# Kernel tuning notes

Measured on AMD Instinct MI355X. Metric: run time of the kernel, lower is better.

## Reference

```python
import jax, jax.numpy as jnp
import numpy as np

H = 1024
V = 32000
L = 15
B = 512


def setup_inputs() -> dict:
    key = jax.random.key(0)
    ks = jax.random.split(key, 16)
    s = 0.02
    return {
        "input_ids": jax.random.randint(ks[0], (B,), 0, V),
        "hidden": jax.random.normal(ks[1], (1, B, H), jnp.float32),
        "encoder_outputs": jax.random.normal(ks[2], (L, B, H), jnp.float32),
        "max_length": L,
        "embedding": jax.random.normal(ks[3], (V, H), jnp.float32) * s,
        "attn1_w": jax.random.normal(ks[4], (1, 2 * H), jnp.float32) * s,
        "attn1_b": jnp.zeros((1,), jnp.float32),
        "combine_w": jax.random.normal(ks[5], (H, 2 * H), jnp.float32) * s,
        "combine_b": jnp.zeros((H,), jnp.float32),
        "w_ih": jax.random.normal(ks[6], (3 * H, H), jnp.float32) * s,
        "w_hh": jax.random.normal(ks[7], (3 * H, H), jnp.float32) * s,
        "b_ih": jnp.zeros((3 * H,), jnp.float32),
        "b_hh": jnp.zeros((3 * H,), jnp.float32),
        "out_w": jax.random.normal(ks[8], (V, H), jnp.float32) * s,
        "out_b": jnp.zeros((V,), jnp.float32),
    }


def reference(input_ids, hidden, encoder_outputs, max_length, embedding,
              attn1_w, attn1_b, combine_w, combine_b,
              w_ih, w_hh, b_ih, b_hh, out_w, out_b):
    # embedding lookup (dropout is identity in eval mode)
    emb = embedding[input_ids]                       # [B, H]
    # Bahdanau-style additive scores: vectorize the per-step python loop
    emb_l = jnp.broadcast_to(emb[None], (max_length, B, H))   # [L, B, H]
    cat = jnp.concatenate([emb_l, encoder_outputs], axis=-1)  # [L, B, 2H]
    scores = cat @ attn1_w.T + attn1_b               # [L, B, 1]
    attn_weights = jax.nn.softmax(scores, axis=0)    # softmax over L
    ctx = jnp.sum(attn_weights * encoder_outputs, axis=0)     # [B, H]
    x = jnp.concatenate([emb, ctx], axis=-1) @ combine_w.T + combine_b  # [B, H]
    # n_layers = 1: relu then one GRU step (seq len 1)
    x = jax.nn.relu(x)
    h = hidden[0]                                    # [B, H]
    gi = x @ w_ih.T + b_ih                           # [B, 3H]
    gh = h @ w_hh.T + b_hh                           # [B, 3H]
    i_r, i_z, i_n = jnp.split(gi, 3, axis=1)
    h_r, h_z, h_n = jnp.split(gh, 3, axis=1)
    r = jax.nn.sigmoid(i_r + h_r)
    z = jax.nn.sigmoid(i_z + h_z)
    n = jnp.tanh(i_n + r * h_n)
    h_new = (1.0 - z) * n + z * h                    # [B, H]
    logits = h_new @ out_w.T + out_b                 # [B, V]
    output = jax.nn.log_softmax(logits, axis=1)
    return output, h_new[None], attn_weights
```

## Files before the change

### kernel.cpp

```cpp
#include <hip/hip_runtime.h>

#define HH 1024
#define VV 32000
#define LL 15
#define BB 512

typedef __bf16 bf16;
typedef __bf16 bf16x4 __attribute__((ext_vector_type(4)));
typedef __bf16 bf16x8 __attribute__((ext_vector_type(8)));
typedef float f32x4 __attribute__((ext_vector_type(4)));

__device__ __forceinline__ unsigned short f2bf(float f) {
    unsigned int u = __float_as_uint(f);
    unsigned int r = (u + 0x7fffu + ((u >> 16) & 1u)) >> 16;
    return (unsigned short)r;
}

__device__ __forceinline__ void gld_lds16(const void* g, void* l) {
    __builtin_amdgcn_global_load_lds(
        (const __attribute__((address_space(1))) unsigned int*)g,
        (__attribute__((address_space(3))) unsigned int*)l, 16, 0, 0);
}

__global__ __launch_bounds__(256)
void cvt4_kernel(const float* __restrict__ a0, unsigned short* __restrict__ o0, int n0_,
                 const float* __restrict__ a1, unsigned short* __restrict__ o1, int n1_,
                 const float* __restrict__ a2, unsigned short* __restrict__ o2, int n2_,
                 const float* __restrict__ a3, unsigned short* __restrict__ o3, int n3_) {
    int i = blockIdx.x * 256 + threadIdx.x;
    const float* src; unsigned short* dst;
    if (i < n0_) { src = a0; dst = o0; }
    else if ((i -= n0_) < n1_) { src = a1; dst = o1; }
    else if ((i -= n1_) < n2_) { src = a2; dst = o2; }
    else if ((i -= n2_) < n3_) { src = a3; dst = o3; }
    else return;
    const f32x4 a = ((const f32x4*)src)[2 * i], b = ((const f32x4*)src)[2 * i + 1];
    ((bf16x4*)dst)[2 * i]     = __builtin_convertvector(a, bf16x4);
    ((bf16x4*)dst)[2 * i + 1] = __builtin_convertvector(b, bf16x4);
}

__global__ __launch_bounds__(256)
void attn_kernel(const int* __restrict__ ids, const float* __restrict__ enc,
                 const float* __restrict__ embedding,
                 const float* __restrict__ attn1_w, const float* __restrict__ attn1_b,
                 float* __restrict__ attn_out, unsigned short* __restrict__ cat_out) {
    const int b = blockIdx.x, tid = threadIdx.x;
    const int lane = tid & 63, wv = tid >> 6;

    __shared__ float s_enc[LL * HH];
    __shared__ float s_scores[LL];
    __shared__ float s_red[4];

    for (int idx = tid; idx < LL * HH / 4; idx += 256) {
        const int l = (idx * 4) >> 10, h = (idx * 4) & (HH - 1);
        *(f32x4*)&s_enc[idx * 4] = *(const f32x4*)&enc[((size_t)l * BB + b) * HH + h];
    }

    const float* embr = embedding + (size_t)ids[b] * HH;
    float p = 0.f;
    for (int j = tid; j < HH; j += 256) p += embr[j] * attn1_w[j];
    #pragma unroll
    for (int o = 32; o; o >>= 1) p += __shfl_xor(p, o);
    if (lane == 0) s_red[wv] = p;
    __syncthreads();
    const float semb = s_red[0] + s_red[1] + s_red[2] + s_red[3] + attn1_b[0];

    for (int l = wv; l < LL; l += 4) {
        float q = 0.f;
        for (int j = lane; j < HH; j += 64) q += s_enc[l * HH + j] * attn1_w[HH + j];
        #pragma unroll
        for (int o = 32; o; o >>= 1) q += __shfl_xor(q, o);
        if (lane == 0) s_scores[l] = q + semb;
    }
    __syncthreads();

    float mx = -3.4e38f;
    #pragma unroll
    for (int l = 0; l < LL; l++) mx = fmaxf(mx, s_scores[l]);
    float aw[LL], sum = 0.f;
    #pragma unroll
    for (int l = 0; l < LL; l++) { aw[l] = __expf(s_scores[l] - mx); sum += aw[l]; }
    const float inv = 1.f / sum;
    #pragma unroll
    for (int l = 0; l < LL; l++) aw[l] *= inv;

    if (tid < LL) attn_out[tid * BB + b] = aw[tid];

    for (int j = tid; j < HH; j += 256) {
        float c = 0.f;
        #pragma unroll
        for (int l = 0; l < LL; l++) c += aw[l] * s_enc[l * HH + j];
        cat_out[(size_t)b * (2 * HH) + j] = f2bf(embr[j]);
        cat_out[(size_t)b * (2 * HH) + HH + j] = f2bf(c);
    }
}

template<int TM, int TN, int OUT, int GATES>
__global__ __launch_bounds__(256)
void gemm_nt(const bf16* __restrict__ A, const bf16* __restrict__ B,
             const float* __restrict__ bias, void* __restrict__ Cout,
             const bf16* __restrict__ A2, const bf16* __restrict__ B2,
             const float* __restrict__ bias2, void* __restrict__ C2,
             const int K, const int N) {
    constexpr int FM = TM / 32, FN = TN / 32;
    __shared__ bf16 As[TM * 64];
    __shared__ bf16 Bs[TN * 64];

    if (GATES && blockIdx.z == 1) { A = A2; B = B2; bias = bias2; Cout = C2; }

    const int tid = threadIdx.x;
    const int lane = tid & 63, wave = tid >> 6;
    const int wm = wave >> 1, wn = wave & 1;
    const int rlo = lane & 15, khi = lane >> 4;
    const int m0 = blockIdx.y * TM, n0 = blockIdx.x * TN;

    f32x4 acc[FM][FN] = {};
    constexpr int IA = TM / 32, IB = TN / 32;

    for (int k0 = 0; k0 < K; k0 += 64) {
        #pragma unroll
        for (int i = 0; i < IA; i++) {
            const int t = (i * 256 + tid) * 8;
            gld_lds16(A + (size_t)(m0 + (t >> 6)) * K + (k0 + (t & 63)), As + i * 2048 + wave * 512);
        }
        #pragma unroll
        for (int i = 0; i < IB; i++) {
            const int t = (i * 256 + tid) * 8;
            gld_lds16(B + (size_t)(n0 + (t >> 6)) * K + (k0 + (t & 63)), Bs + i * 2048 + wave * 512);
        }
        __syncthreads();

        bf16x8 af[FM][2], bfr[FN][2];
        #pragma unroll
        for (int m = 0; m < FM; m++)
            #pragma unroll
            for (int ks = 0; ks < 2; ks++)
                af[m][ks] = *(const bf16x8*)(As + (wm * (TM / 2) + m * 16 + rlo) * 64 + ks * 32 + khi * 8);
        #pragma unroll
        for (int n = 0; n < FN; n++)
            #pragma unroll
            for (int ks = 0; ks < 2; ks++)
                bfr[n][ks] = *(const bf16x8*)(Bs + (wn * (TN / 2) + n * 16 + rlo) * 64 + ks * 32 + khi * 8);
        #pragma unroll
        for (int ks = 0; ks < 2; ks++)
            #pragma unroll
            for (int m = 0; m < FM; m++)
                #pragma unroll
                for (int n = 0; n < FN; n++)
                    acc[m][n] = __builtin_amdgcn_mfma_f32_16x16x32_bf16(af[m][ks], bfr[n][ks], acc[m][n], 0, 0, 0);
        __syncthreads();
    }

    #pragma unroll
    for (int m = 0; m < FM; m++) {
        const int gr = m0 + wm * (TM / 2) + m * 16 + khi * 4;
        #pragma unroll
        for (int n = 0; n < FN; n++) {
            const int gc = n0 + wn * (TN / 2) + n * 16 + rlo;
            const float bv = bias[gc];
            #pragma unroll
            for (int j = 0; j < 4; j++) {
                float v = acc[m][n][j] + bv;
                if (OUT == 1) {
                    v = fmaxf(v, 0.f);
                    ((unsigned short*)Cout)[(size_t)(gr + j) * N + gc] = f2bf(v);
                } else {
                    ((float*)Cout)[(size_t)(gr + j) * N + gc] = v;
                }
            }
        }
    }
}

__global__ __launch_bounds__(256, 3)
void gemm_out(const bf16* __restrict__ A, const float* __restrict__ B,
              const float* __restrict__ bias, float* __restrict__ C,
              float* __restrict__ pmax, float* __restrict__ psum) {
    constexpr int K = HH, N = VV;
    __shared__ bf16 As[128 * 64];
    __shared__ bf16 Bs[64 * 64];
    __shared__ float sPm[2][128], sPs[2][128];

    const int tid = threadIdx.x;
    const int lane = tid & 63, wave = tid >> 6;
    const int wm = wave >> 1, wn = wave & 1;
    const int rlo = lane & 15, khi = lane >> 4;

    constexpr int gridN = VV / 64;
    constexpr int nFull = (gridN >> 3) << 5;
    const int bidx = blockIdx.x;
    int g, jm;
    if (bidx < nFull) { const int s = bidx >> 5, rem = bidx & 31; jm = rem >> 3; g = s * 8 + (rem & 7); }
    else { const int rem = bidx - nFull; constexpr int gleft = gridN & 7; g = (gridN & ~7) + rem % gleft; jm = rem / gleft; }
    const int n0 = g * 64, m0 = jm * 128;

    f32x4 acc[4][2] = {};

    for (int k0 = 0; k0 < K; k0 += 64) {
        f32x4 bv[4];
        #pragma unroll
        for (int i = 0; i < 4; i++) {
            const int idx = i * 256 + tid;
            const int row = idx >> 4, c4 = idx & 15;
            bv[i] = *(const f32x4*)(B + (size_t)(n0 + row) * K + k0 + c4 * 4);
        }
        #pragma unroll
        for (int i = 0; i < 4; i++) {
            const int p = (i * 256 + tid) * 16;
            const int row = p >> 7;
            const int qs = (p & 127) ^ ((row & 7) << 4);
            gld_lds16(A + (size_t)(m0 + row) * K + k0 + (qs >> 1),
                      As + i * 2048 + wave * 512);
        }
        #pragma unroll
        for (int i = 0; i < 4; i++) {
            const int idx = i * 256 + tid;
            const int row = idx >> 4, c4 = idx & 15;
            bf16x4 w = __builtin_convertvector(bv[i], bf16x4);
            *(bf16x4*)((char*)Bs + row * 128 + ((c4 * 8) ^ ((row & 7) << 4))) = w;
        }
        __syncthreads();

        #pragma unroll
        for (int ks = 0; ks < 2; ks++) {
            bf16x8 af[4], bfr[2];
            #pragma unroll
            for (int m = 0; m < 4; m++) {
                const int r = wm * 64 + m * 16 + rlo;
                const int sw = (ks * 64 + khi * 16) ^ ((r & 7) << 4);
                af[m] = *(const bf16x8*)((const char*)As + r * 128 + sw);
            }
            #pragma unroll
            for (int n = 0; n < 2; n++) {
                const int r = wn * 32 + n * 16 + rlo;
                const int sw = (ks * 64 + khi * 16) ^ ((r & 7) << 4);
                bfr[n] = *(const bf16x8*)((const char*)Bs + r * 128 + sw);
            }
            #pragma unroll
            for (int m = 0; m < 4; m++)
                #pragma unroll
                for (int n = 0; n < 2; n++)
                    acc[m][n] = __builtin_amdgcn_mfma_f32_16x16x32_bf16(af[m], bfr[n], acc[m][n], 0, 0, 0);
        }
        __syncthreads();
    }

    float bvn[2];
    #pragma unroll
    for (int n = 0; n < 2; n++) bvn[n] = bias[n0 + wn * 32 + n * 16 + rlo];

    #pragma unroll
    for (int m = 0; m < 4; m++) {
        const int rbase = wm * 64 + m * 16 + khi * 4;
        #pragma unroll
        for (int j = 0; j < 4; j++) {
            const int gr = m0 + rbase + j;
            float v[2];
            #pragma unroll
            for (int n = 0; n < 2; n++) {
                v[n] = acc[m][n][j] + bvn[n];
                C[(size_t)gr * N + n0 + wn * 32 + n * 16 + rlo] = v[n];
            }
            float lm = fmaxf(v[0], v[1]);
            #pragma unroll
            for (int o = 8; o; o >>= 1) lm = fmaxf(lm, __shfl_xor(lm, o));
            float ls = __expf(v[0] - lm) + __expf(v[1] - lm);
            #pragma unroll
            for (int o = 8; o; o >>= 1) ls += __shfl_xor(ls, o);
            if (rlo == 0) { sPm[wn][rbase + j] = lm; sPs[wn][rbase + j] = ls; }
        }
    }
    __syncthreads();
    if (tid < 128) {
        const float ma = sPm[0][tid], mb = sPm[1][tid];
        const float M = fmaxf(ma, mb);
        const float S = sPs[0][tid] * __expf(ma - M) + sPs[1][tid] * __expf(mb - M);
        pmax[(size_t)(m0 + tid) * 512 + g] = M;
        psum[(size_t)(m0 + tid) * 512 + g] = S;
    }
}

__global__ __launch_bounds__(256)
void gru_kernel(const float* __restrict__ gi, const float* __restrict__ gh,
                const float* __restrict__ h, float* __restrict__ hnew,
                unsigned short* __restrict__ hnew_bf) {
    const int i = blockIdx.x * 256 + threadIdx.x;
    const int e = i * 4;
    const int b = e >> 10, j = e & (HH - 1);
    const size_t o = ((size_t)b * 3 * HH + j) / 4;
    const f32x4 ir = ((const f32x4*)gi)[o],          iz = ((const f32x4*)gi)[o + HH / 4],
                in_ = ((const f32x4*)gi)[o + 2 * HH / 4];
    const f32x4 hr = ((const f32x4*)gh)[o],          hz = ((const f32x4*)gh)[o + HH / 4],
                hn = ((const f32x4*)gh)[o + 2 * HH / 4];
    const f32x4 hv = ((const f32x4*)h)[i];
    f32x4 out;
    ushort4 ob;
    #pragma unroll
    for (int c = 0; c < 4; c++) {
        const float r = 1.f / (1.f + __expf(-(ir[c] + hr[c])));
        const float z = 1.f / (1.f + __expf(-(iz[c] + hz[c])));
        const float n = tanhf(in_[c] + r * hn[c]);
        const float v = (1.f - z) * n + z * hv[c];
        out[c] = v;
        ((unsigned short*)&ob)[c] = f2bf(v);
    }
    ((f32x4*)hnew)[i] = out;
    ((ushort4*)hnew_bf)[i] = ob;
}

__global__ __launch_bounds__(512)
void lsm_final(const float* __restrict__ pmax, const float* __restrict__ psum,
               float* __restrict__ logits) {
    const int b = blockIdx.x, tid = threadIdx.x;
    const int lane = tid & 63, wv = tid >> 6;
    __shared__ float sm[8], ss[8];

    float m = -3.4e38f, s = 0.f;
    if (tid < VV / 64) { m = pmax[(size_t)b * 512 + tid]; s = psum[(size_t)b * 512 + tid]; }
    #pragma unroll
    for (int o = 32; o; o >>= 1) {
        const float mo = __shfl_xor(m, o), so = __shfl_xor(s, o);
        const float nm = fmaxf(m, mo);
        s = s * __expf(m - nm) + so * __expf(mo - nm);
        m = nm;
    }
    if (lane == 0) { sm[wv] = m; ss[wv] = s; }
    __syncthreads();
    float M = sm[0], S;
    #pragma unroll
    for (int w = 1; w < 8; w++) M = fmaxf(M, sm[w]);
    S = ss[0] * __expf(sm[0] - M);
    #pragma unroll
    for (int w = 1; w < 8; w++) S += ss[w] * __expf(sm[w] - M);
    const float lse = M + __logf(S);

    float* row = logits + (size_t)b * VV;
    for (int j = tid; j < VV / 4; j += 512) {
        f32x4 v = ((const f32x4*)row)[j];
        v[0] -= lse; v[1] -= lse; v[2] -= lse; v[3] -= lse;
        ((f32x4*)row)[j] = v;
    }
}

extern "C" void kernel_launch(void* const* d_in, const int* in_sizes, int n_in,
                              void* d_out, int out_size, void* d_ws, size_t ws_size,
                              hipStream_t stream) {
    const int*   ids       = (const int*)d_in[0];
    const float* hidden    = (const float*)d_in[1];
    const float* enc       = (const float*)d_in[2];
    const float* embedding = (const float*)d_in[4];
    const float* attn1_w   = (const float*)d_in[5];
    const float* attn1_b   = (const float*)d_in[6];
    const float* combine_w = (const float*)d_in[7];
    const float* combine_b = (const float*)d_in[8];
    const float* w_ih      = (const float*)d_in[9];
    const float* w_hh      = (const float*)d_in[10];
    const float* b_ih      = (const float*)d_in[11];
    const float* b_hh      = (const float*)d_in[12];
    const float* out_w     = (const float*)d_in[13];
    const float* out_b     = (const float*)d_in[14];

    float* out_lsm = (float*)d_out;
    float* out_h   = out_lsm + (size_t)BB * VV;
    float* out_aw  = out_h + (size_t)BB * HH;

    char* w = (char*)d_ws;
    unsigned short* w_ih_bf  = (unsigned short*)w;   w += (size_t)3 * HH * HH * 2;
    unsigned short* w_hh_bf  = (unsigned short*)w;   w += (size_t)3 * HH * HH * 2;
    unsigned short* w_cb_bf  = (unsigned short*)w;   w += (size_t)2 * HH * HH * 2;
    unsigned short* cat_bf   = (unsigned short*)w;   w += (size_t)BB * 2 * HH * 2;
    unsigned short* x_bf     = (unsigned short*)w;   w += (size_t)BB * HH * 2;
    unsigned short* hid_bf   = (unsigned short*)w;   w += (size_t)BB * HH * 2;
    unsigned short* hnew_bf  = (unsigned short*)w;   w += (size_t)BB * HH * 2;
    float* gi   = (float*)w;                         w += (size_t)BB * 3 * HH * 4;
    float* gh   = (float*)w;                         w += (size_t)BB * 3 * HH * 4;
    float* pmax = (float*)w;                         w += (size_t)BB * 512 * 4;
    float* psum = (float*)w;                         w += (size_t)BB * 512 * 4;

    cvt4_kernel<<<(3 * HH * HH / 8 * 2 + 2 * HH * HH / 8 + BB * HH / 8) / 256, 256, 0, stream>>>(
        w_ih, w_ih_bf, 3 * HH * HH / 8,
        w_hh, w_hh_bf, 3 * HH * HH / 8,
        combine_w, w_cb_bf, 2 * HH * HH / 8,
        hidden, hid_bf, BB * HH / 8);

    attn_kernel<<<BB, 256, 0, stream>>>(ids, enc, embedding, attn1_w, attn1_b, out_aw, cat_bf);

    gemm_nt<64, 64, 1, 0><<<dim3(HH / 64, BB / 64), 256, 0, stream>>>(
        (const bf16*)cat_bf, (const bf16*)w_cb_bf, combine_b, x_bf,
        nullptr, nullptr, nullptr, nullptr, 2 * HH, HH);

    gemm_nt<64, 64, 0, 1><<<dim3(3 * HH / 64, BB / 64, 2), 256, 0, stream>>>(
        (const bf16*)hid_bf, (const bf16*)w_hh_bf, b_hh, gh,
        (const bf16*)x_bf, (const bf16*)w_ih_bf, b_ih, gi, HH, 3 * HH);

    gru_kernel<<<(BB * HH / 4) / 256, 256, 0, stream>>>(gi, gh, hidden, out_h, hnew_bf);

    gemm_out<<<(VV / 64) * 4, 256, 0, stream>>>(
        (const bf16*)hnew_bf, out_w, out_b, out_lsm, pmax, psum);

    lsm_final<<<BB, 512, 0, stream>>>(pmax, psum, out_lsm);
}
```

Measured before the change: 183.0 us.

## Double-buffer LDS tiles in gemm_nt and gemm_out to overlap loads with MFMA

Both GEMM kernels now use two LDS buffers per operand, so the next K-tile is prefetched while the current tile is being multiplied. This cuts the loop to one barrier per iteration. gemm_out also register-prefetches its fp32 B tile two steps ahead and converts it to bf16 after compute. gemm_nt additionally switches its A/B LDS layout to an XOR swizzle to reduce bank conflicts. The cost is doubled LDS use and more registers, which may lower occupancy (gemm_out keeps launch bounds of 3 blocks).

```diff
diff --git a/kernel.cpp b/kernel.cpp
--- a/kernel.cpp
+++ b/kernel.cpp
@@ -103,8 +103,8 @@
              const float* __restrict__ bias2, void* __restrict__ C2,
              const int K, const int N) {
     constexpr int FM = TM / 32, FN = TN / 32;
-    __shared__ bf16 As[TM * 64];
-    __shared__ bf16 Bs[TN * 64];
+    __shared__ bf16 As[2][TM * 64];
+    __shared__ bf16 Bs[2][TN * 64];
 
     if (GATES && blockIdx.z == 1) { A = A2; B = B2; bias = bias2; Cout = C2; }
 
@@ -117,38 +117,58 @@
     f32x4 acc[FM][FN] = {};
     constexpr int IA = TM / 32, IB = TN / 32;
 
-    for (int k0 = 0; k0 < K; k0 += 64) {
+    auto stage = [&](int k0, int buf) {
         #pragma unroll
         for (int i = 0; i < IA; i++) {
-            const int t = (i * 256 + tid) * 8;
-            gld_lds16(A + (size_t)(m0 + (t >> 6)) * K + (k0 + (t & 63)), As + i * 2048 + wave * 512);
+            const int p = (i * 256 + tid) * 16;
+            const int row = p >> 7;
+            const int qs = (p & 127) ^ ((row & 7) << 4);
+            gld_lds16(A + (size_t)(m0 + row) * K + k0 + (qs >> 1),
+                      &As[buf][0] + i * 2048 + wave * 512);
         }
         #pragma unroll
         for (int i = 0; i < IB; i++) {
-            const int t = (i * 256 + tid) * 8;
-            gld_lds16(B + (size_t)(n0 + (t >> 6)) * K + (k0 + (t & 63)), Bs + i * 2048 + wave * 512);
-        }
-        __syncthreads();
-
-        bf16x8 af[FM][2], bfr[FN][2];
-        #pragma unroll
-        for (int m = 0; m < FM; m++)
-            #pragma unroll
-            for (int ks = 0; ks < 2; ks++)
-                af[m][ks] = *(const bf16x8*)(As + (wm * (TM / 2) + m * 16 + rlo) * 64 + ks * 32 + khi * 8);
-        #pragma unroll
-        for (int n = 0; n < FN; n++)
-            #pragma unroll
-            for (int ks = 0; ks < 2; ks++)
-                bfr[n][ks] = *(const bf16x8*)(Bs + (wn * (TN / 2) + n * 16 + rlo) * 64 + ks * 32 + khi * 8);
-        #pragma unroll
-        for (int ks = 0; ks < 2; ks++)
+            const int p = (i * 256 + tid) * 16;
+            const int row = p >> 7;
+            const int qs = (p & 127) ^ ((row & 7) << 4);
+            gld_lds16(B + (size_t)(n0 + row) * K + k0 + (qs >> 1),
+                      &Bs[buf][0] + i * 2048 + wave * 512);
+        }
+    };
+
+    auto compute = [&](int buf) {
+        #pragma unroll
+        for (int ks = 0; ks < 2; ks++) {
+            bf16x8 af[FM], bfr[FN];
+            #pragma unroll
+            for (int m = 0; m < FM; m++) {
+                const int r = wm * (TM / 2) + m * 16 + rlo;
+                const int sw = (ks * 64 + khi * 16) ^ ((r & 7) << 4);
+                af[m] = *(const bf16x8*)((const char*)&As[buf][0] + r * 128 + sw);
+            }
+            #pragma unroll
+            for (int n = 0; n < FN; n++) {
+                const int r = wn * (TN / 2) + n * 16 + rlo;
+                const int sw = (ks * 64 + khi * 16) ^ ((r & 7) << 4);
+                bfr[n] = *(const bf16x8*)((const char*)&Bs[buf][0] + r * 128 + sw);
+            }
             #pragma unroll
             for (int m = 0; m < FM; m++)
                 #pragma unroll
                 for (int n = 0; n < FN; n++)
-                    acc[m][n] = __builtin_amdgcn_mfma_f32_16x16x32_bf16(af[m][ks], bfr[n][ks], acc[m][n], 0, 0, 0);
+                    acc[m][n] = __builtin_amdgcn_mfma_f32_16x16x32_bf16(af[m], bfr[n], acc[m][n], 0, 0, 0);
+        }
+    };
+
+    stage(0, 0);
+    __syncthreads();
+    int cur = 0;
+    const int NT = K >> 6;
+    for (int kt = 0; kt < NT; kt++) {
+        if (kt + 1 < NT) stage((kt + 1) << 6, cur ^ 1);
+        compute(cur);
         __syncthreads();
+        cur ^= 1;
     }
 
     #pragma unroll
@@ -177,8 +197,8 @@
               const float* __restrict__ bias, float* __restrict__ C,
               float* __restrict__ pmax, float* __restrict__ psum) {
     constexpr int K = HH, N = VV;
-    __shared__ bf16 As[128 * 64];
-    __shared__ bf16 Bs[64 * 64];
+    __shared__ bf16 As[2][128 * 64];
+    __shared__ bf16 Bs[2][64 * 64];
     __shared__ float sPm[2][128], sPs[2][128];
 
     const int tid = threadIdx.x;
@@ -195,32 +215,36 @@
     const int n0 = g * 64, m0 = jm * 128;
 
     f32x4 acc[4][2] = {};
-
-    for (int k0 = 0; k0 < K; k0 += 64) {
-        f32x4 bv[4];
+    f32x4 bvA[4], bvB[4];
+
+    auto loadB = [&](int k0, f32x4* bv) {
         #pragma unroll
         for (int i = 0; i < 4; i++) {
             const int idx = i * 256 + tid;
             const int row = idx >> 4, c4 = idx & 15;
             bv[i] = *(const f32x4*)(B + (size_t)(n0 + row) * K + k0 + c4 * 4);
         }
+    };
+    auto stageA = [&](int k0, int buf) {
         #pragma unroll
         for (int i = 0; i < 4; i++) {
             const int p = (i * 256 + tid) * 16;
             const int row = p >> 7;
             const int qs = (p & 127) ^ ((row & 7) << 4);
             gld_lds16(A + (size_t)(m0 + row) * K + k0 + (qs >> 1),
-                      As + i * 2048 + wave * 512);
-        }
+                      &As[buf][0] + i * 2048 + wave * 512);
+        }
+    };
+    auto writeB = [&](const f32x4* bv, int buf) {
         #pragma unroll
         for (int i = 0; i < 4; i++) {
             const int idx = i * 256 + tid;
             const int row = idx >> 4, c4 = idx & 15;
             bf16x4 w = __builtin_convertvector(bv[i], bf16x4);
-            *(bf16x4*)((char*)Bs + row * 128 + ((c4 * 8) ^ ((row & 7) << 4))) = w;
-        }
-        __syncthreads();
-
+            *(bf16x4*)((char*)&Bs[buf][0] + row * 128 + ((c4 * 8) ^ ((row & 7) << 4))) = w;
+        }
+    };
+    auto compute = [&](int buf) {
         #pragma unroll
         for (int ks = 0; ks < 2; ks++) {
             bf16x8 af[4], bfr[2];
@@ -228,13 +252,13 @@
             for (int m = 0; m < 4; m++) {
                 const int r = wm * 64 + m * 16 + rlo;
                 const int sw = (ks * 64 + khi * 16) ^ ((r & 7) << 4);
-                af[m] = *(const bf16x8*)((const char*)As + r * 128 + sw);
+                af[m] = *(const bf16x8*)((const char*)&As[buf][0] + r * 128 + sw);
             }
             #pragma unroll
             for (int n = 0; n < 2; n++) {
                 const int r = wn * 32 + n * 16 + rlo;
                 const int sw = (ks * 64 + khi * 16) ^ ((r & 7) << 4);
-                bfr[n] = *(const bf16x8*)((const char*)Bs + r * 128 + sw);
+                bfr[n] = *(const bf16x8*)((const char*)&Bs[buf][0] + r * 128 + sw);
             }
             #pragma unroll
             for (int m = 0; m < 4; m++)
@@ -242,7 +266,34 @@
                 for (int n = 0; n < 2; n++)
                     acc[m][n] = __builtin_amdgcn_mfma_f32_16x16x32_bf16(af[m], bfr[n], acc[m][n], 0, 0, 0);
         }
-        __syncthreads();
+    };
+
+    loadB(0, bvA);
+    stageA(0, 0);
+    writeB(bvA, 0);
+    loadB(64, bvA);
+    __syncthreads();
+
+    int cur = 0;
+    for (int kt = 0; kt < 16; kt += 2) {
+        {
+            const int k1 = (kt + 1) << 6, k2 = (kt + 2) << 6;
+            if (k1 < K) stageA(k1, cur ^ 1);
+            if (k2 < K) loadB(k2, bvB);
+            compute(cur);
+            if (k1 < K) writeB(bvA, cur ^ 1);
+            __syncthreads();
+            cur ^= 1;
+        }
+        {
+            const int k2 = (kt + 2) << 6, k3 = (kt + 3) << 6;
+            if (k2 < K) stageA(k2, cur ^ 1);
+            if (k3 < K) loadB(k3, bvA);
+            compute(cur);
+            if (k2 < K) writeB(bvB, cur ^ 1);
+            __syncthreads();
+            cur ^= 1;
+        }
     }
 
     float bvn[2];
```

After: 183.8 us. About the same (+0.4%).
